# Kernel tuning notes

Hardware: AMD Instinct MI355X
Metric: run time of the kernel (lower is better)

## Reference

```python
import jax, jax.numpy as jnp
import numpy as np
from jax import lax

B, H, W, C = 8, 256, 256, 64
REDUCTION = 8
LENGTH = 9
HIDDEN = max(8, C // REDUCTION)


def _conv(x, w, b, pad='SAME'):
    y = lax.conv_general_dilated(x, w, (1, 1), pad,
                                 dimension_numbers=('NHWC', 'HWIO', 'NHWC'))
    return y + b


def _bilinear_sample(img, y, x):
    # img: [B,H,W,C]; y,x: [B,H,W] float coords
    Bi, Hi, Wi, _ = img.shape
    y0 = jnp.floor(y)
    x0 = jnp.floor(x)
    y0i = jnp.clip(y0.astype(jnp.int32), 0, Hi - 1)
    x0i = jnp.clip(x0.astype(jnp.int32), 0, Wi - 1)
    y1i = jnp.clip((y0 + 1.0).astype(jnp.int32), 0, Hi - 1)
    x1i = jnp.clip((x0 + 1.0).astype(jnp.int32), 0, Wi - 1)
    b = jnp.arange(Bi)[:, None, None]
    Ia = img[b, y0i, x0i]
    Ib = img[b, y1i, x0i]
    Ic = img[b, y0i, x1i]
    Id = img[b, y1i, x1i]
    # weights use CLIPPED integer corner coords (faithful to the TF source)
    y0f = y0i.astype(img.dtype)
    x0f = x0i.astype(img.dtype)
    y1f = y1i.astype(img.dtype)
    x1f = x1i.astype(img.dtype)
    wa = ((x1f - x) * (y1f - y))[..., None]
    wb = ((x1f - x) * (y - y0f))[..., None]
    wc = ((x - x0f) * (y1f - y))[..., None]
    wd = ((x - x0f) * (y - y0f))[..., None]
    return wa * Ia + wb * Ib + wc * Ic + wd * Id


def _oriented_pool(x, vx, vy):
    # x: [B,H,W,C]; vx,vy: [B,H,W] unit direction components
    _, Hi, Wi, _ = x.shape
    yy = jnp.arange(Hi, dtype=x.dtype)[None, :, None]  # broadcasts to [B,H,W]
    xx = jnp.arange(Wi, dtype=x.dtype)[None, None, :]
    half = LENGTH // 2
    acc = jnp.zeros_like(x)
    for t in range(-half, half + 1):  # fixed small set of offsets
        tf_ = jnp.asarray(t, dtype=x.dtype)
        cy = yy + tf_ * vy
        cx = xx + tf_ * vx
        acc = acc + _bilinear_sample(x, cy, cx)
    return acc / jnp.asarray(LENGTH, dtype=x.dtype)


def setup_inputs() -> dict:
    key = jax.random.key(0)
    ks = jax.random.split(key, 9)
    s = 0.05
    return {
        'x': jax.random.normal(ks[0], (B, H, W, C), jnp.float32),
        'w3': jax.random.normal(ks[1], (3, 3, C, HIDDEN), jnp.float32) * s,
        'b3': jnp.zeros((HIDDEN,), jnp.float32),
        'w1': jax.random.normal(ks[2], (1, 1, HIDDEN, 1), jnp.float32) * s,
        'b1': jnp.zeros((1,), jnp.float32),
        'wr': jax.random.normal(ks[3], (1, 1, 2 * C, HIDDEN), jnp.float32) * s,
        'br': jnp.zeros((HIDDEN,), jnp.float32),
        'we': jax.random.normal(ks[4], (1, 1, HIDDEN, 2 * C), jnp.float32) * s,
        'be': jnp.zeros((2 * C,), jnp.float32),
    }


def reference(x, w3, b3, w1, b1, wr, br, we, be):
    h = jax.nn.relu(_conv(x, w3, b3))                    # [B,H,W,hidden]
    theta = np.pi * jax.nn.sigmoid(_conv(h, w1, b1))     # [B,H,W,1]
    cos_t = jnp.cos(theta)[..., 0]                       # [B,H,W]
    sin_t = jnp.sin(theta)[..., 0]
    tan_feat = _oriented_pool(x, cos_t, sin_t)           # tangential direction
    nor_feat = _oriented_pool(x, -sin_t, cos_t)          # normal direction
    context = jnp.concatenate([tan_feat, nor_feat], axis=-1)  # [B,H,W,2C]
    r = jax.nn.relu(_conv(context, wr, br))
    w = jax.nn.sigmoid(_conv(r, we, be))                 # [B,H,W,2C]
    alpha_tan, alpha_norm = jnp.split(w, 2, axis=-1)
    return (alpha_tan + alpha_norm) * x
```

## Files before the change

### kernel.cpp

```cpp
#include <hip/hip_runtime.h>
#include <math.h>

#define Bq 8
#define Hq 256
#define Wq 256
#define Cq 64
#define HID 8
#define PI_F 3.14159265358979323846f

__device__ __forceinline__ float fold8(float v0, float v1, float v2, float v3,
                                       float v4, float v5, float v6, float v7,
                                       int lane) {
    const bool b4 = (lane & 4) != 0;
    float k0 = b4 ? v4 : v0, g0 = b4 ? v0 : v4;
    float k1 = b4 ? v5 : v1, g1 = b4 ? v1 : v5;
    float k2 = b4 ? v6 : v2, g2 = b4 ? v2 : v6;
    float k3 = b4 ? v7 : v3, g3 = b4 ? v3 : v7;
    k0 += __shfl_xor(g0, 4, 64);
    k1 += __shfl_xor(g1, 4, 64);
    k2 += __shfl_xor(g2, 4, 64);
    k3 += __shfl_xor(g3, 4, 64);
    const bool b2 = (lane & 2) != 0;
    float m0 = b2 ? k2 : k0, n0 = b2 ? k0 : k2;
    float m1 = b2 ? k3 : k1, n1 = b2 ? k1 : k3;
    m0 += __shfl_xor(n0, 2, 64);
    m1 += __shfl_xor(n1, 2, 64);
    const bool b1_ = (lane & 1) != 0;
    float q = b1_ ? m1 : m0, r = b1_ ? m0 : m1;
    q += __shfl_xor(r, 1, 64);
    q += __shfl_xor(q, 8, 64);
    q += __shfl_xor(q, 16, 64);
    q += __shfl_xor(q, 32, 64);
    return q;
}

__device__ __forceinline__ float bilin_s(const float* __restrict__ img,
                                         float cy, float cx, int lane) {
    float fy0 = floorf(cy);
    float fx0 = floorf(cx);
    int y0 = __builtin_amdgcn_readfirstlane((int)fy0);
    int x0 = __builtin_amdgcn_readfirstlane((int)fx0);
    int y0i = min(max(y0, 0), Hq - 1);
    int x0i = min(max(x0, 0), Wq - 1);
    int y1i = min(max(y0 + 1, 0), Hq - 1);
    int x1i = min(max(x0 + 1, 0), Wq - 1);
    float wy0 = (float)y1i - cy;
    float wy1 = cy - (float)y0i;
    float wx0 = (float)x1i - cx;
    float wx1 = cx - (float)x0i;
    const float* pa = img + (size_t)(((y0i << 8) + x0i) << 6);
    const float* pb = img + (size_t)(((y1i << 8) + x0i) << 6);
    const float* pc = img + (size_t)(((y0i << 8) + x1i) << 6);
    const float* pd = img + (size_t)(((y1i << 8) + x1i) << 6);
    float Ia = pa[lane], Ib = pb[lane], Ic = pc[lane], Id = pd[lane];
    return (wx0 * wy0) * Ia + (wx0 * wy1) * Ib + (wx1 * wy0) * Ic + (wx1 * wy1) * Id;
}

__global__ __launch_bounds__(256) void oca_kernel(
    const float* __restrict__ x,
    const float* __restrict__ w3, const float* __restrict__ b3,
    const float* __restrict__ w1, const float* __restrict__ b1,
    const float* __restrict__ wr, const float* __restrict__ br,
    const float* __restrict__ we, const float* __restrict__ be,
    float* __restrict__ out) {
    const int lane = threadIdx.x & 63;
    const int wid = __builtin_amdgcn_readfirstlane(blockIdx.x * 4 + (threadIdx.x >> 6));
    const int b  = wid >> 16;
    const int yq = (wid >> 8) & 255;
    const int xq = wid & 255;
    const float* img = x + ((size_t)b << 22);

    float h0 = 0.f, h1 = 0.f, h2 = 0.f, h3 = 0.f;
    float h4 = 0.f, h5 = 0.f, h6 = 0.f, h7 = 0.f;
#pragma unroll
    for (int dy = -1; dy <= 1; ++dy) {
        int yy = yq + dy;
        if ((unsigned)yy >= (unsigned)Hq) continue;
#pragma unroll
        for (int dx = -1; dx <= 1; ++dx) {
            int xx = xq + dx;
            if ((unsigned)xx >= (unsigned)Wq) continue;
            float xv = img[(size_t)(((yy << 8) + xx) << 6) + lane];
            const float* wp = w3 + (size_t)((((dy + 1) * 3 + dx + 1) << 6) + lane) * HID;
            float4 wv0 = *(const float4*)(wp);
            float4 wv1 = *(const float4*)(wp + 4);
            h0 = fmaf(xv, wv0.x, h0);
            h1 = fmaf(xv, wv0.y, h1);
            h2 = fmaf(xv, wv0.z, h2);
            h3 = fmaf(xv, wv0.w, h3);
            h4 = fmaf(xv, wv1.x, h4);
            h5 = fmaf(xv, wv1.y, h5);
            h6 = fmaf(xv, wv1.z, h6);
            h7 = fmaf(xv, wv1.w, h7);
        }
    }
    const int j = lane & 7;
    float hsum = fold8(h0, h1, h2, h3, h4, h5, h6, h7, lane);
    float h_l = fmaxf(hsum + b3[j], 0.f);

    float zp = h_l * w1[j];
    zp += __shfl_xor(zp, 1, 64);
    zp += __shfl_xor(zp, 2, 64);
    zp += __shfl_xor(zp, 4, 64);
    float z = zp + b1[0];
    float theta = PI_F * __builtin_amdgcn_rcpf(1.f + __expf(-z));
    float ct = __cosf(theta);
    float st = __sinf(theta);

    const float fy = (float)yq, fx = (float)xq;
    float acc_t = 0.f, acc_n = 0.f;
#pragma unroll
    for (int t = -4; t <= 4; ++t) {
        float tf = (float)t;
        acc_t += bilin_s(img, fmaf(tf, st, fy), fmaf(tf, ct, fx), lane);
        acc_n += bilin_s(img, fmaf(tf, ct, fy), fmaf(-tf, st, fx), lane);
    }
    float tanv = acc_t * (1.f / 9.f);
    float norv = acc_n * (1.f / 9.f);

    const float* wrp0 = wr + (size_t)lane * HID;
    const float* wrp1 = wr + (size_t)(64 + lane) * HID;
    float4 a0 = *(const float4*)(wrp0);
    float4 a1 = *(const float4*)(wrp0 + 4);
    float4 c0 = *(const float4*)(wrp1);
    float4 c1 = *(const float4*)(wrp1 + 4);
    float p0 = fmaf(tanv, a0.x, norv * c0.x);
    float p1 = fmaf(tanv, a0.y, norv * c0.y);
    float p2 = fmaf(tanv, a0.z, norv * c0.z);
    float p3 = fmaf(tanv, a0.w, norv * c0.w);
    float p4 = fmaf(tanv, a1.x, norv * c1.x);
    float p5 = fmaf(tanv, a1.y, norv * c1.y);
    float p6 = fmaf(tanv, a1.z, norv * c1.z);
    float p7 = fmaf(tanv, a1.w, norv * c1.w);
    float rsum = fold8(p0, p1, p2, p3, p4, p5, p6, p7, lane);
    float r_l = fmaxf(rsum + br[j], 0.f);

    float rb0 = r_l;
    float rb1 = __shfl_xor(rb0, 1, 64);
    float rb2 = __shfl_xor(rb0, 2, 64);
    float rb3 = __shfl_xor(rb1, 2, 64);
    float rb4 = __shfl_xor(rb0, 4, 64);
    float rb5 = __shfl_xor(rb1, 4, 64);
    float rb6 = __shfl_xor(rb2, 4, 64);
    float rb7 = __shfl_xor(rb3, 4, 64);

    const float* web = we + ((size_t)j << 7) + lane;
    float zt = be[lane];
    float zn = be[64 + lane];
    zt = fmaf(rb0, web[0],            zt); zn = fmaf(rb0, web[64],            zn);
    zt = fmaf(rb1, *(const float*)((uintptr_t)web ^ (1u << 9)),        zt);
    zn = fmaf(rb1, *(const float*)(((uintptr_t)web ^ (1u << 9)) + 256), zn);
    zt = fmaf(rb2, *(const float*)((uintptr_t)web ^ (2u << 9)),        zt);
    zn = fmaf(rb2, *(const float*)(((uintptr_t)web ^ (2u << 9)) + 256), zn);
    zt = fmaf(rb3, *(const float*)((uintptr_t)web ^ (3u << 9)),        zt);
    zn = fmaf(rb3, *(const float*)(((uintptr_t)web ^ (3u << 9)) + 256), zn);
    zt = fmaf(rb4, *(const float*)((uintptr_t)web ^ (4u << 9)),        zt);
    zn = fmaf(rb4, *(const float*)(((uintptr_t)web ^ (4u << 9)) + 256), zn);
    zt = fmaf(rb5, *(const float*)((uintptr_t)web ^ (5u << 9)),        zt);
    zn = fmaf(rb5, *(const float*)(((uintptr_t)web ^ (5u << 9)) + 256), zn);
    zt = fmaf(rb6, *(const float*)((uintptr_t)web ^ (6u << 9)),        zt);
    zn = fmaf(rb6, *(const float*)(((uintptr_t)web ^ (6u << 9)) + 256), zn);
    zt = fmaf(rb7, *(const float*)((uintptr_t)web ^ (7u << 9)),        zt);
    zn = fmaf(rb7, *(const float*)(((uintptr_t)web ^ (7u << 9)) + 256), zn);

    float wt = __builtin_amdgcn_rcpf(1.f + __expf(-zt));
    float wn = __builtin_amdgcn_rcpf(1.f + __expf(-zn));
    float xc = img[(size_t)(((yq << 8) + xq) << 6) + lane];
    out[((size_t)wid << 6) + lane] = (wt + wn) * xc;
}

extern "C" void kernel_launch(void* const* d_in, const int* in_sizes, int n_in,
                              void* d_out, int out_size, void* d_ws, size_t ws_size,
                              hipStream_t stream) {
    const float* x  = (const float*)d_in[0];
    const float* w3 = (const float*)d_in[1];
    const float* b3 = (const float*)d_in[2];
    const float* w1 = (const float*)d_in[3];
    const float* b1 = (const float*)d_in[4];
    const float* wr = (const float*)d_in[5];
    const float* br = (const float*)d_in[6];
    const float* we = (const float*)d_in[7];
    const float* be = (const float*)d_in[8];
    float* out = (float*)d_out;

    const int total_waves = Bq * Hq * Wq;
    dim3 grid(total_waves / 4), block(256);
    oca_kernel<<<grid, block, 0, stream>>>(x, w3, b3, w1, b1, wr, br, we, be, out);
}
```

Before: 913.8 us.

## Process two pixels per wave with float2 channel pairs and packed FMAs

Each wavefront now handles two adjacent pixels, with each 32-lane half owning one pixel and each lane holding two channels as a float2. Loads become 8-byte vector loads, the math uses packed FMA, and the tap loop drops its branches in favour of clamp-and-select. A small pre-kernel repacks w3 and wr into a channel-pair layout in the workspace, and the final shuffle stage of the reduction is dropped. The aim is to halve the wave count, cut per-pixel instruction overhead, and reduce scalar address work. The cost is an extra launch, and the bilinear coordinates are no longer wave-uniform, so gathers become divergent vector loads.

Measured after the change: 1.322 ms. 44.7% more time.

```diff
diff --git a/kernel.cpp b/kernel.cpp
--- a/kernel.cpp
+++ b/kernel.cpp
@@ -8,10 +8,21 @@
 #define HID 8
 #define PI_F 3.14159265358979323846f
 
-__device__ __forceinline__ float fold8(float v0, float v1, float v2, float v3,
-                                       float v4, float v5, float v6, float v7,
-                                       int lane) {
-    const bool b4 = (lane & 4) != 0;
+typedef float f2 __attribute__((ext_vector_type(2)));
+
+__device__ __forceinline__ f2 pkfma(f2 a, f2 b, f2 c) {
+#if __has_builtin(__builtin_elementwise_fma)
+    return __builtin_elementwise_fma(a, b, c);
+#else
+    f2 r; r.x = fmaf(a.x, b.x, c.x); r.y = fmaf(a.y, b.y, c.y); return r;
+#endif
+}
+__device__ __forceinline__ f2 sp(float v) { f2 r; r.x = v; r.y = v; return r; }
+
+__device__ __forceinline__ float fold8h(float v0, float v1, float v2, float v3,
+                                        float v4, float v5, float v6, float v7,
+                                        int hl) {
+    const bool b4 = (hl & 4) != 0;
     float k0 = b4 ? v4 : v0, g0 = b4 ? v0 : v4;
     float k1 = b4 ? v5 : v1, g1 = b4 ? v1 : v5;
     float k2 = b4 ? v6 : v2, g2 = b4 ? v2 : v6;
@@ -20,82 +31,112 @@
     k1 += __shfl_xor(g1, 4, 64);
     k2 += __shfl_xor(g2, 4, 64);
     k3 += __shfl_xor(g3, 4, 64);
-    const bool b2 = (lane & 2) != 0;
+    const bool b2 = (hl & 2) != 0;
     float m0 = b2 ? k2 : k0, n0 = b2 ? k0 : k2;
     float m1 = b2 ? k3 : k1, n1 = b2 ? k1 : k3;
     m0 += __shfl_xor(n0, 2, 64);
     m1 += __shfl_xor(n1, 2, 64);
-    const bool b1_ = (lane & 1) != 0;
+    const bool b1_ = (hl & 1) != 0;
     float q = b1_ ? m1 : m0, r = b1_ ? m0 : m1;
     q += __shfl_xor(r, 1, 64);
     q += __shfl_xor(q, 8, 64);
     q += __shfl_xor(q, 16, 64);
-    q += __shfl_xor(q, 32, 64);
     return q;
 }
 
-__device__ __forceinline__ float bilin_s(const float* __restrict__ img,
-                                         float cy, float cx, int lane) {
-    float fy0 = floorf(cy);
-    float fx0 = floorf(cx);
-    int y0 = __builtin_amdgcn_readfirstlane((int)fy0);
-    int x0 = __builtin_amdgcn_readfirstlane((int)fx0);
+__device__ __forceinline__ void bilin2(const char* __restrict__ xb, unsigned laneoff,
+                                       float cy, float cx, f2& acc) {
+    float fy0 = floorf(cy), fx0 = floorf(cx);
+    int y0 = (int)fy0, x0 = (int)fx0;
     int y0i = min(max(y0, 0), Hq - 1);
+    int y1i = min(max(y0 + 1, 0), Hq - 1);
     int x0i = min(max(x0, 0), Wq - 1);
-    int y1i = min(max(y0 + 1, 0), Hq - 1);
     int x1i = min(max(x0 + 1, 0), Wq - 1);
-    float wy0 = (float)y1i - cy;
-    float wy1 = cy - (float)y0i;
-    float wx0 = (float)x1i - cx;
-    float wx1 = cx - (float)x0i;
-    const float* pa = img + (size_t)(((y0i << 8) + x0i) << 6);
-    const float* pb = img + (size_t)(((y1i << 8) + x0i) << 6);
-    const float* pc = img + (size_t)(((y0i << 8) + x1i) << 6);
-    const float* pd = img + (size_t)(((y1i << 8) + x1i) << 6);
-    float Ia = pa[lane], Ib = pb[lane], Ic = pc[lane], Id = pd[lane];
-    return (wx0 * wy0) * Ia + (wx0 * wy1) * Ib + (wx1 * wy0) * Ic + (wx1 * wy1) * Id;
+    float wy0 = (float)y1i - cy, wy1 = cy - (float)y0i;
+    float wx0 = (float)x1i - cx, wx1 = cx - (float)x0i;
+    unsigned r0 = ((unsigned)y0i << 16) + laneoff;
+    unsigned r1 = ((unsigned)y1i << 16) + laneoff;
+    unsigned c0 = (unsigned)x0i << 8, c1 = (unsigned)x1i << 8;
+    f2 Ia = *(const f2*)(xb + (r0 + c0));
+    f2 Ib = *(const f2*)(xb + (r1 + c0));
+    f2 Ic = *(const f2*)(xb + (r0 + c1));
+    f2 Id = *(const f2*)(xb + (r1 + c1));
+    acc = pkfma(sp(wx0 * wy0), Ia, acc);
+    acc = pkfma(sp(wx0 * wy1), Ib, acc);
+    acc = pkfma(sp(wx1 * wy0), Ic, acc);
+    acc = pkfma(sp(wx1 * wy1), Id, acc);
+}
+
+__global__ void repack_kernel(const float* __restrict__ w3,
+                              const float* __restrict__ wr,
+                              f2* __restrict__ ws) {
+    int t = blockIdx.x * 256 + threadIdx.x;
+    if (t < 2304) {
+        int tap = t >> 8, rem = t & 255, hl = rem >> 3, j = rem & 7;
+        f2 v; v.x = w3[((tap << 6) + (hl << 1)) * 8 + j];
+        v.y = w3[((tap << 6) + (hl << 1) + 1) * 8 + j];
+        ws[t] = v;
+    } else if (t < 2560) {
+        int rem = t - 2304, hl = rem >> 3, j = rem & 7;
+        f2 v; v.x = wr[(hl << 1) * 8 + j];
+        v.y = wr[((hl << 1) + 1) * 8 + j];
+        ws[t] = v;
+    } else if (t < 2816) {
+        int rem = t - 2560, hl = rem >> 3, j = rem & 7;
+        f2 v; v.x = wr[(64 + (hl << 1)) * 8 + j];
+        v.y = wr[(64 + (hl << 1) + 1) * 8 + j];
+        ws[t] = v;
+    }
 }
 
 __global__ __launch_bounds__(256) void oca_kernel(
     const float* __restrict__ x,
-    const float* __restrict__ w3, const float* __restrict__ b3,
-    const float* __restrict__ w1, const float* __restrict__ b1,
-    const float* __restrict__ wr, const float* __restrict__ br,
+    const float* __restrict__ b3, const float* __restrict__ w1,
+    const float* __restrict__ b1, const float* __restrict__ br,
     const float* __restrict__ we, const float* __restrict__ be,
+    const f2* __restrict__ ws,
     float* __restrict__ out) {
     const int lane = threadIdx.x & 63;
-    const int wid = __builtin_amdgcn_readfirstlane(blockIdx.x * 4 + (threadIdx.x >> 6));
-    const int b  = wid >> 16;
-    const int yq = (wid >> 8) & 255;
-    const int xq = wid & 255;
-    const float* img = x + ((size_t)b << 22);
-
-    float h0 = 0.f, h1 = 0.f, h2 = 0.f, h3 = 0.f;
-    float h4 = 0.f, h5 = 0.f, h6 = 0.f, h7 = 0.f;
+    const int hl = lane & 31;
+    const int half = lane >> 5;
+    const int w = __builtin_amdgcn_readfirstlane(blockIdx.x * 4 + (threadIdx.x >> 6));
+    const int b   = w >> 15;
+    const int yq  = (w >> 7) & 255;
+    const int xq0 = (2 * w) & 255;
+    const int xql = xq0 + half;
+    const char* xb = (const char*)(x + ((size_t)b << 22));
+    const unsigned laneoff = (unsigned)hl << 3;
+
+    f2 a0 = sp(0.f), a1 = sp(0.f), a2 = sp(0.f), a3 = sp(0.f);
+    f2 a4 = sp(0.f), a5 = sp(0.f), a6 = sp(0.f), a7 = sp(0.f);
+    f2 xc2 = sp(0.f);
 #pragma unroll
     for (int dy = -1; dy <= 1; ++dy) {
-        int yy = yq + dy;
-        if ((unsigned)yy >= (unsigned)Hq) continue;
 #pragma unroll
         for (int dx = -1; dx <= 1; ++dx) {
-            int xx = xq + dx;
-            if ((unsigned)xx >= (unsigned)Wq) continue;
-            float xv = img[(size_t)(((yy << 8) + xx) << 6) + lane];
-            const float* wp = w3 + (size_t)((((dy + 1) * 3 + dx + 1) << 6) + lane) * HID;
-            float4 wv0 = *(const float4*)(wp);
-            float4 wv1 = *(const float4*)(wp + 4);
-            h0 = fmaf(xv, wv0.x, h0);
-            h1 = fmaf(xv, wv0.y, h1);
-            h2 = fmaf(xv, wv0.z, h2);
-            h3 = fmaf(xv, wv0.w, h3);
-            h4 = fmaf(xv, wv1.x, h4);
-            h5 = fmaf(xv, wv1.y, h5);
-            h6 = fmaf(xv, wv1.z, h6);
-            h7 = fmaf(xv, wv1.w, h7);
+            int yy = yq + dy;
+            int xx = xql + dx;
+            int yyc = min(max(yy, 0), Hq - 1);
+            int xxc = min(max(xx, 0), Wq - 1);
+            bool valid = ((unsigned)yy < (unsigned)Hq) && ((unsigned)xx < (unsigned)Wq);
+            f2 xv = *(const f2*)(xb + (((unsigned)yyc << 16) + ((unsigned)xxc << 8) + laneoff));
+            xv = valid ? xv : sp(0.f);
+            if (dy == 0 && dx == 0) xc2 = xv;
+            const int tap = (dy + 1) * 3 + (dx + 1);
+            const f2* wp = ws + (tap << 8) + (hl << 3);
+            a0 = pkfma(xv, wp[0], a0);
+            a1 = pkfma(xv, wp[1], a1);
+            a2 = pkfma(xv, wp[2], a2);
+            a3 = pkfma(xv, wp[3], a3);
+            a4 = pkfma(xv, wp[4], a4);
+            a5 = pkfma(xv, wp[5], a5);
+            a6 = pkfma(xv, wp[6], a6);
+            a7 = pkfma(xv, wp[7], a7);
         }
     }
-    const int j = lane & 7;
-    float hsum = fold8(h0, h1, h2, h3, h4, h5, h6, h7, lane);
+    const int j = hl & 7;
+    float hsum = fold8h(a0.x + a0.y, a1.x + a1.y, a2.x + a2.y, a3.x + a3.y,
+                        a4.x + a4.y, a5.x + a5.y, a6.x + a6.y, a7.x + a7.y, hl);
     float h_l = fmaxf(hsum + b3[j], 0.f);
 
     float zp = h_l * w1[j];
@@ -107,32 +148,29 @@
     float ct = __cosf(theta);
     float st = __sinf(theta);
 
-    const float fy = (float)yq, fx = (float)xq;
-    float acc_t = 0.f, acc_n = 0.f;
+    const float fy = (float)yq, fx = (float)xql;
+    f2 acc_t = sp(0.f), acc_n = sp(0.f);
 #pragma unroll
     for (int t = -4; t <= 4; ++t) {
         float tf = (float)t;
-        acc_t += bilin_s(img, fmaf(tf, st, fy), fmaf(tf, ct, fx), lane);
-        acc_n += bilin_s(img, fmaf(tf, ct, fy), fmaf(-tf, st, fx), lane);
-    }
-    float tanv = acc_t * (1.f / 9.f);
-    float norv = acc_n * (1.f / 9.f);
-
-    const float* wrp0 = wr + (size_t)lane * HID;
-    const float* wrp1 = wr + (size_t)(64 + lane) * HID;
-    float4 a0 = *(const float4*)(wrp0);
-    float4 a1 = *(const float4*)(wrp0 + 4);
-    float4 c0 = *(const float4*)(wrp1);
-    float4 c1 = *(const float4*)(wrp1 + 4);
-    float p0 = fmaf(tanv, a0.x, norv * c0.x);
-    float p1 = fmaf(tanv, a0.y, norv * c0.y);
-    float p2 = fmaf(tanv, a0.z, norv * c0.z);
-    float p3 = fmaf(tanv, a0.w, norv * c0.w);
-    float p4 = fmaf(tanv, a1.x, norv * c1.x);
-    float p5 = fmaf(tanv, a1.y, norv * c1.y);
-    float p6 = fmaf(tanv, a1.z, norv * c1.z);
-    float p7 = fmaf(tanv, a1.w, norv * c1.w);
-    float rsum = fold8(p0, p1, p2, p3, p4, p5, p6, p7, lane);
+        bilin2(xb, laneoff, fmaf(tf, st, fy), fmaf(tf, ct, fx), acc_t);
+        bilin2(xb, laneoff, fmaf(tf, ct, fy), fmaf(-tf, st, fx), acc_n);
+    }
+    f2 tan2; tan2.x = acc_t.x * (1.f / 9.f); tan2.y = acc_t.y * (1.f / 9.f);
+    f2 nor2; nor2.x = acc_n.x * (1.f / 9.f); nor2.y = acc_n.y * (1.f / 9.f);
+
+    const f2* wrp = ws + 2304 + (hl << 3);
+    const f2* wrn = ws + 2560 + (hl << 3);
+    f2 p0 = pkfma(tan2, wrp[0], sp(0.f)); p0 = pkfma(nor2, wrn[0], p0);
+    f2 p1 = pkfma(tan2, wrp[1], sp(0.f)); p1 = pkfma(nor2, wrn[1], p1);
+    f2 p2 = pkfma(tan2, wrp[2], sp(0.f)); p2 = pkfma(nor2, wrn[2], p2);
+    f2 p3 = pkfma(tan2, wrp[3], sp(0.f)); p3 = pkfma(nor2, wrn[3], p3);
+    f2 p4 = pkfma(tan2, wrp[4], sp(0.f)); p4 = pkfma(nor2, wrn[4], p4);
+    f2 p5 = pkfma(tan2, wrp[5], sp(0.f)); p5 = pkfma(nor2, wrn[5], p5);
+    f2 p6 = pkfma(tan2, wrp[6], sp(0.f)); p6 = pkfma(nor2, wrn[6], p6);
+    f2 p7 = pkfma(tan2, wrp[7], sp(0.f)); p7 = pkfma(nor2, wrn[7], p7);
+    float rsum = fold8h(p0.x + p0.y, p1.x + p1.y, p2.x + p2.y, p3.x + p3.y,
+                        p4.x + p4.y, p5.x + p5.y, p6.x + p6.y, p7.x + p7.y, hl);
     float r_l = fmaxf(rsum + br[j], 0.f);
 
     float rb0 = r_l;
@@ -144,29 +182,27 @@
     float rb6 = __shfl_xor(rb2, 4, 64);
     float rb7 = __shfl_xor(rb3, 4, 64);
 
-    const float* web = we + ((size_t)j << 7) + lane;
-    float zt = be[lane];
-    float zn = be[64 + lane];
-    zt = fmaf(rb0, web[0],            zt); zn = fmaf(rb0, web[64],            zn);
-    zt = fmaf(rb1, *(const float*)((uintptr_t)web ^ (1u << 9)),        zt);
-    zn = fmaf(rb1, *(const float*)(((uintptr_t)web ^ (1u << 9)) + 256), zn);
-    zt = fmaf(rb2, *(const float*)((uintptr_t)web ^ (2u << 9)),        zt);
-    zn = fmaf(rb2, *(const float*)(((uintptr_t)web ^ (2u << 9)) + 256), zn);
-    zt = fmaf(rb3, *(const float*)((uintptr_t)web ^ (3u << 9)),        zt);
-    zn = fmaf(rb3, *(const float*)(((uintptr_t)web ^ (3u << 9)) + 256), zn);
-    zt = fmaf(rb4, *(const float*)((uintptr_t)web ^ (4u << 9)),        zt);
-    zn = fmaf(rb4, *(const float*)(((uintptr_t)web ^ (4u << 9)) + 256), zn);
-    zt = fmaf(rb5, *(const float*)((uintptr_t)web ^ (5u << 9)),        zt);
-    zn = fmaf(rb5, *(const float*)(((uintptr_t)web ^ (5u << 9)) + 256), zn);
-    zt = fmaf(rb6, *(const float*)((uintptr_t)web ^ (6u << 9)),        zt);
-    zn = fmaf(rb6, *(const float*)(((uintptr_t)web ^ (6u << 9)) + 256), zn);
-    zt = fmaf(rb7, *(const float*)((uintptr_t)web ^ (7u << 9)),        zt);
-    zn = fmaf(rb7, *(const float*)(((uintptr_t)web ^ (7u << 9)) + 256), zn);
-
-    float wt = __builtin_amdgcn_rcpf(1.f + __expf(-zt));
-    float wn = __builtin_amdgcn_rcpf(1.f + __expf(-zn));
-    float xc = img[(size_t)(((yq << 8) + xq) << 6) + lane];
-    out[((size_t)wid << 6) + lane] = (wt + wn) * xc;
+    const char* web = (const char*)we;
+    unsigned voff = ((unsigned)j << 9) | laneoff;
+    f2 zt2 = *(const f2*)((const char*)be + laneoff);
+    f2 zn2 = *(const f2*)((const char*)be + 256 + laneoff);
+#pragma unroll
+    for (int m = 0; m < 8; ++m) {
+        unsigned vm = voff ^ ((unsigned)m << 9);
+        float rbm = (m == 0) ? rb0 : (m == 1) ? rb1 : (m == 2) ? rb2 : (m == 3) ? rb3
+                  : (m == 4) ? rb4 : (m == 5) ? rb5 : (m == 6) ? rb6 : rb7;
+        zt2 = pkfma(sp(rbm), *(const f2*)(web + vm), zt2);
+        zn2 = pkfma(sp(rbm), *(const f2*)(web + vm + 256), zn2);
+    }
+    f2 wt2, wn2;
+    wt2.x = __builtin_amdgcn_rcpf(1.f + __expf(-zt2.x));
+    wt2.y = __builtin_amdgcn_rcpf(1.f + __expf(-zt2.y));
+    wn2.x = __builtin_amdgcn_rcpf(1.f + __expf(-zn2.x));
+    wn2.y = __builtin_amdgcn_rcpf(1.f + __expf(-zn2.y));
+
+    f2 g; g.x = wt2.x + wn2.x; g.y = wt2.y + wn2.y;
+    f2 o; o.x = g.x * xc2.x;   o.y = g.y * xc2.y;
+    *(f2*)((char*)out + (((size_t)w) << 9) + ((unsigned)lane << 3)) = o;
 }
 
 extern "C" void kernel_launch(void* const* d_in, const int* in_sizes, int n_in,
@@ -182,8 +218,11 @@
     const float* we = (const float*)d_in[7];
     const float* be = (const float*)d_in[8];
     float* out = (float*)d_out;
-
-    const int total_waves = Bq * Hq * Wq;
+    f2* ws = (f2*)d_ws;
+
+    repack_kernel<<<11, 256, 0, stream>>>(w3, wr, ws);
+
+    const int total_waves = Bq * Hq * Wq / 2;
     dim3 grid(total_waves / 4), block(256);
-    oca_kernel<<<grid, block, 0, stream>>>(x, w3, b3, w1, b1, wr, br, we, be, out);
-}
+    oca_kernel<<<grid, block, 0, stream>>>(x, b3, w1, b1, br, we, be, ws, out);
+}
```

## Add interior fast path skipping clamps and reusing center pixel

Applied to the files above, without the earlier changes.

Wavefronts whose pixel lies at least five pixels from the border take a specialised path. It drops bounds checks and clamping in the 3x3 conv and in the bilinear sampler, and derives the four corner addresses from one base pointer with fixed offsets. The center pixel loaded for the conv is reused for the t=0 sample of both oriented pools and for the final output multiply, removing redundant loads. Border pixels keep the original clamped path. The cost is extra code size and a divergent branch per block.

Measured after the change: 955.4 us. 4.6% more time.

```diff
diff --git a/kernel.cpp b/kernel.cpp
--- a/kernel.cpp
+++ b/kernel.cpp
@@ -1,11 +1,6 @@
 #include <hip/hip_runtime.h>
 #include <math.h>
 
-#define Bq 8
-#define Hq 256
-#define Wq 256
-#define Cq 64
-#define HID 8
 #define PI_F 3.14159265358979323846f
 
 __device__ __forceinline__ float fold8(float v0, float v1, float v2, float v3,
@@ -40,10 +35,10 @@
     float fx0 = floorf(cx);
     int y0 = __builtin_amdgcn_readfirstlane((int)fy0);
     int x0 = __builtin_amdgcn_readfirstlane((int)fx0);
-    int y0i = min(max(y0, 0), Hq - 1);
-    int x0i = min(max(x0, 0), Wq - 1);
-    int y1i = min(max(y0 + 1, 0), Hq - 1);
-    int x1i = min(max(x0 + 1, 0), Wq - 1);
+    int y0i = min(max(y0, 0), 255);
+    int x0i = min(max(x0, 0), 255);
+    int y1i = min(max(y0 + 1, 0), 255);
+    int x1i = min(max(x0 + 1, 0), 255);
     float wy0 = (float)y1i - cy;
     float wy1 = cy - (float)y0i;
     float wx0 = (float)x1i - cx;
@@ -53,6 +48,24 @@
     const float* pc = img + (size_t)(((y0i << 8) + x1i) << 6);
     const float* pd = img + (size_t)(((y1i << 8) + x1i) << 6);
     float Ia = pa[lane], Ib = pb[lane], Ic = pc[lane], Id = pd[lane];
+    return (wx0 * wy0) * Ia + (wx0 * wy1) * Ib + (wx1 * wy0) * Ic + (wx1 * wy1) * Id;
+}
+
+__device__ __forceinline__ float bilin_f(const float* __restrict__ img,
+                                         float cy, float cx, int lane) {
+    float fy = floorf(cy), fx = floorf(cx);
+    int y0 = __builtin_amdgcn_readfirstlane((int)fy);
+    int x0 = __builtin_amdgcn_readfirstlane((int)fx);
+    float wy1 = cy - fy;
+    float wy0 = (fy + 1.f) - cy;
+    float wx1 = cx - fx;
+    float wx0 = (fx + 1.f) - cx;
+    const float* p00 = img + (size_t)(((y0 << 8) + x0) << 6);
+    const float* p10 = p00 + (1 << 14);
+    float Ia = p00[lane];
+    float Ib = p10[lane];
+    float Ic = p00[lane + 64];
+    float Id = p10[lane + 64];
     return (wx0 * wy0) * Ia + (wx0 * wy1) * Ib + (wx1 * wy0) * Ic + (wx1 * wy1) * Id;
 }
 
@@ -70,28 +83,55 @@
     const int xq = wid & 255;
     const float* img = x + ((size_t)b << 22);
 
+    const bool inner = (yq >= 5) && (yq <= 250) && (xq >= 5) && (xq <= 250);
+
     float h0 = 0.f, h1 = 0.f, h2 = 0.f, h3 = 0.f;
     float h4 = 0.f, h5 = 0.f, h6 = 0.f, h7 = 0.f;
-#pragma unroll
-    for (int dy = -1; dy <= 1; ++dy) {
-        int yy = yq + dy;
-        if ((unsigned)yy >= (unsigned)Hq) continue;
-#pragma unroll
-        for (int dx = -1; dx <= 1; ++dx) {
-            int xx = xq + dx;
-            if ((unsigned)xx >= (unsigned)Wq) continue;
-            float xv = img[(size_t)(((yy << 8) + xx) << 6) + lane];
-            const float* wp = w3 + (size_t)((((dy + 1) * 3 + dx + 1) << 6) + lane) * HID;
-            float4 wv0 = *(const float4*)(wp);
-            float4 wv1 = *(const float4*)(wp + 4);
-            h0 = fmaf(xv, wv0.x, h0);
-            h1 = fmaf(xv, wv0.y, h1);
-            h2 = fmaf(xv, wv0.z, h2);
-            h3 = fmaf(xv, wv0.w, h3);
-            h4 = fmaf(xv, wv1.x, h4);
-            h5 = fmaf(xv, wv1.y, h5);
-            h6 = fmaf(xv, wv1.z, h6);
-            h7 = fmaf(xv, wv1.w, h7);
+    float xc = 0.f;
+    if (inner) {
+        const float* base = img + (size_t)((((yq - 1) << 8) + (xq - 1)) << 6);
+#pragma unroll
+        for (int dy = 0; dy < 3; ++dy) {
+#pragma unroll
+            for (int dx = 0; dx < 3; ++dx) {
+                float xv = base[(dy << 14) + (dx << 6) + lane];
+                if (dy == 1 && dx == 1) xc = xv;
+                const float* wp = w3 + (size_t)(((dy * 3 + dx) << 6) + lane) * 8;
+                float4 w0 = *(const float4*)(wp);
+                float4 w1v = *(const float4*)(wp + 4);
+                h0 = fmaf(xv, w0.x, h0);
+                h1 = fmaf(xv, w0.y, h1);
+                h2 = fmaf(xv, w0.z, h2);
+                h3 = fmaf(xv, w0.w, h3);
+                h4 = fmaf(xv, w1v.x, h4);
+                h5 = fmaf(xv, w1v.y, h5);
+                h6 = fmaf(xv, w1v.z, h6);
+                h7 = fmaf(xv, w1v.w, h7);
+            }
+        }
+    } else {
+#pragma unroll
+        for (int dy = -1; dy <= 1; ++dy) {
+            int yy = yq + dy;
+            if ((unsigned)yy >= 256u) continue;
+#pragma unroll
+            for (int dx = -1; dx <= 1; ++dx) {
+                int xx = xq + dx;
+                if ((unsigned)xx >= 256u) continue;
+                float xv = img[(size_t)(((yy << 8) + xx) << 6) + lane];
+                if (dy == 0 && dx == 0) xc = xv;
+                const float* wp = w3 + (size_t)((((dy + 1) * 3 + dx + 1) << 6) + lane) * 8;
+                float4 w0 = *(const float4*)(wp);
+                float4 w1v = *(const float4*)(wp + 4);
+                h0 = fmaf(xv, w0.x, h0);
+                h1 = fmaf(xv, w0.y, h1);
+                h2 = fmaf(xv, w0.z, h2);
+                h3 = fmaf(xv, w0.w, h3);
+                h4 = fmaf(xv, w1v.x, h4);
+                h5 = fmaf(xv, w1v.y, h5);
+                h6 = fmaf(xv, w1v.z, h6);
+                h7 = fmaf(xv, w1v.w, h7);
+            }
         }
     }
     const int j = lane & 7;
@@ -108,18 +148,32 @@
     float st = __sinf(theta);
 
     const float fy = (float)yq, fx = (float)xq;
-    float acc_t = 0.f, acc_n = 0.f;
-#pragma unroll
-    for (int t = -4; t <= 4; ++t) {
-        float tf = (float)t;
-        acc_t += bilin_s(img, fmaf(tf, st, fy), fmaf(tf, ct, fx), lane);
-        acc_n += bilin_s(img, fmaf(tf, ct, fy), fmaf(-tf, st, fx), lane);
+    float acc_t, acc_n;
+    if (inner) {
+        acc_t = xc;
+        acc_n = xc;
+#pragma unroll
+        for (int t = -4; t <= 4; ++t) {
+            if (t == 0) continue;
+            float tf = (float)t;
+            acc_t += bilin_f(img, fmaf(tf, st, fy), fmaf(tf, ct, fx), lane);
+            acc_n += bilin_f(img, fmaf(tf, ct, fy), fmaf(-tf, st, fx), lane);
+        }
+    } else {
+        acc_t = 0.f;
+        acc_n = 0.f;
+#pragma unroll
+        for (int t = -4; t <= 4; ++t) {
+            float tf = (float)t;
+            acc_t += bilin_s(img, fmaf(tf, st, fy), fmaf(tf, ct, fx), lane);
+            acc_n += bilin_s(img, fmaf(tf, ct, fy), fmaf(-tf, st, fx), lane);
+        }
     }
     float tanv = acc_t * (1.f / 9.f);
     float norv = acc_n * (1.f / 9.f);
 
-    const float* wrp0 = wr + (size_t)lane * HID;
-    const float* wrp1 = wr + (size_t)(64 + lane) * HID;
+    const float* wrp0 = wr + (size_t)lane * 8;
+    const float* wrp1 = wr + (size_t)(64 + lane) * 8;
     float4 a0 = *(const float4*)(wrp0);
     float4 a1 = *(const float4*)(wrp0 + 4);
     float4 c0 = *(const float4*)(wrp1);
@@ -144,28 +198,28 @@
     float rb6 = __shfl_xor(rb2, 4, 64);
     float rb7 = __shfl_xor(rb3, 4, 64);
 
-    const float* web = we + ((size_t)j << 7) + lane;
+    const char* web = (const char*)we + ((unsigned)j << 9) + ((unsigned)lane << 2);
     float zt = be[lane];
     float zn = be[64 + lane];
-    zt = fmaf(rb0, web[0],            zt); zn = fmaf(rb0, web[64],            zn);
-    zt = fmaf(rb1, *(const float*)((uintptr_t)web ^ (1u << 9)),        zt);
+    zt = fmaf(rb0, *(const float*)(web), zt);
+    zn = fmaf(rb0, *(const float*)(web + 256), zn);
+    zt = fmaf(rb1, *(const float*)((uintptr_t)web ^ (1u << 9)), zt);
     zn = fmaf(rb1, *(const float*)(((uintptr_t)web ^ (1u << 9)) + 256), zn);
-    zt = fmaf(rb2, *(const float*)((uintptr_t)web ^ (2u << 9)),        zt);
+    zt = fmaf(rb2, *(const float*)((uintptr_t)web ^ (2u << 9)), zt);
     zn = fmaf(rb2, *(const float*)(((uintptr_t)web ^ (2u << 9)) + 256), zn);
-    zt = fmaf(rb3, *(const float*)((uintptr_t)web ^ (3u << 9)),        zt);
+    zt = fmaf(rb3, *(const float*)((uintptr_t)web ^ (3u << 9)), zt);
     zn = fmaf(rb3, *(const float*)(((uintptr_t)web ^ (3u << 9)) + 256), zn);
-    zt = fmaf(rb4, *(const float*)((uintptr_t)web ^ (4u << 9)),        zt);
+    zt = fmaf(rb4, *(const float*)((uintptr_t)web ^ (4u << 9)), zt);
     zn = fmaf(rb4, *(const float*)(((uintptr_t)web ^ (4u << 9)) + 256), zn);
-    zt = fmaf(rb5, *(const float*)((uintptr_t)web ^ (5u << 9)),        zt);
+    zt = fmaf(rb5, *(const float*)((uintptr_t)web ^ (5u << 9)), zt);
     zn = fmaf(rb5, *(const float*)(((uintptr_t)web ^ (5u << 9)) + 256), zn);
-    zt = fmaf(rb6, *(const float*)((uintptr_t)web ^ (6u << 9)),        zt);
+    zt = fmaf(rb6, *(const float*)((uintptr_t)web ^ (6u << 9)), zt);
     zn = fmaf(rb6, *(const float*)(((uintptr_t)web ^ (6u << 9)) + 256), zn);
-    zt = fmaf(rb7, *(const float*)((uintptr_t)web ^ (7u << 9)),        zt);
+    zt = fmaf(rb7, *(const float*)((uintptr_t)web ^ (7u << 9)), zt);
     zn = fmaf(rb7, *(const float*)(((uintptr_t)web ^ (7u << 9)) + 256), zn);
 
     float wt = __builtin_amdgcn_rcpf(1.f + __expf(-zt));
     float wn = __builtin_amdgcn_rcpf(1.f + __expf(-zn));
-    float xc = img[(size_t)(((yq << 8) + xq) << 6) + lane];
     out[((size_t)wid << 6) + lane] = (wt + wn) * xc;
 }
 
@@ -183,7 +237,7 @@
     const float* be = (const float*)d_in[8];
     float* out = (float*)d_out;
 
-    const int total_waves = Bq * Hq * Wq;
+    const int total_waves = 8 * 256 * 256;
     dim3 grid(total_waves / 4), block(256);
     oca_kernel<<<grid, block, 0, stream>>>(x, w3, b3, w1, b1, wr, br, we, be, out);
 }
```
